# Kernel optimization log

Hardware: AMD Instinct MI355X
Metric: run time of the kernel (lower is better)

## Reference

```python
import jax, jax.numpy as jnp
import numpy as np

K = 3            # kernel_size
H = 2048
W = 2048
N = 1_000_000    # number of query points
LATENT = 4
POS = 6
CTRL = 2
HID = 64
OUT = 4
IN_CH = (LATENT + POS + CTRL) * K * K  # 108


def _linear_params(key, fan_in, fan_out):
    bound = 1.0 / np.sqrt(fan_in)
    kw, kb = jax.random.split(key)
    Wm = jax.random.uniform(kw, (fan_in, fan_out), minval=-bound, maxval=bound, dtype=jnp.float32)
    bm = jax.random.uniform(kb, (fan_out,), minval=-bound, maxval=bound, dtype=jnp.float32)
    return Wm, bm


def setup_inputs() -> dict:
    key = jax.random.key(0)
    ks = jax.random.split(key, 7)
    W1, b1 = _linear_params(ks[0], IN_CH, HID)
    W2, b2 = _linear_params(ks[1], HID, 2 * HID)
    W3, b3 = _linear_params(ks[2], 2 * HID, HID)
    W4, b4 = _linear_params(ks[3], HID, OUT)
    latent = jax.random.normal(ks[4], (H, W, LATENT), dtype=jnp.float32)
    raw_pos = jax.random.randint(ks[5], (N, 2), 0, W).astype(jnp.int32)  # (x, y) coords
    control = jax.random.normal(ks[6], (N, CTRL), dtype=jnp.float32)
    return {"latent": latent, "raw_pos": raw_pos, "control": control,
            "W1": W1, "b1": b1, "W2": W2, "b2": b2,
            "W3": W3, "b3": b3, "W4": W4, "b4": b4}


def reference(latent, raw_pos, control, W1, b1, W2, b2, W3, b3, W4, b4):
    Hh, Ww, C = latent.shape
    n = raw_pos.shape[0]
    r = K // 2
    d = jnp.arange(-r, r + 1, dtype=raw_pos.dtype)
    ox, oy = jnp.meshgrid(d, d, indexing="xy")
    offsets = jnp.stack([ox.ravel(), oy.ravel()], axis=-1)          # [K*K, 2] (dx, dy)
    exp = raw_pos[:, None, :] + offsets[None, :, :]                 # [N, K*K, 2]
    ex = jnp.clip(exp[..., 0], 0, Ww - 1)
    ey = jnp.clip(exp[..., 1], 0, Hh - 1)
    lin = ey * Ww + ex                                              # linear gather indices
    latent_values = latent.reshape(-1, C)[lin]                      # [N, K*K, C] irregular gather

    xs = jnp.clip(raw_pos[:, 0:1], 0, Ww - 1).astype(latent.dtype) / Ww
    ys = jnp.clip(raw_pos[:, 1:2], 0, Hh - 1).astype(latent.dtype) / Hh
    tp = jnp.asarray(2.0 * np.pi, latent.dtype)
    # sinusoidal encoding with input included: [x, y, sin(2pi x), cos(2pi x), sin(2pi y), cos(2pi y)] -> pos_channels=6
    pos = jnp.concatenate([xs, ys, jnp.sin(tp * xs), jnp.cos(tp * xs), jnp.sin(tp * ys), jnp.cos(tp * ys)], axis=-1)
    pos_e = jnp.broadcast_to(pos[:, None, :], (n, K * K, POS))
    ctl_e = jnp.broadcast_to(control[:, None, :], (n, K * K, control.shape[-1]))

    patches = jnp.concatenate([latent_values, pos_e, ctl_e], axis=-1)  # [N, K*K, 12]
    x = patches.reshape(n, -1)                                          # [N, 108]

    h = jax.nn.gelu(x @ W1 + b1, approximate=False)
    h = jax.nn.gelu(h @ W2 + b2, approximate=False)
    h = jax.nn.gelu(h @ W3 + b3, approximate=False)
    return jax.nn.sigmoid(h @ W4 + b4)                                  # [N, 4]
```

## Files before the change

### kernel.cpp

```cpp
#include <hip/hip_runtime.h>
#include <hip/hip_fp16.h>

typedef __attribute__((ext_vector_type(8))) _Float16 half8;
typedef __attribute__((ext_vector_type(4))) float f32x4;

#define HGT 2048
#define WID 2048
#define NPTS 1000000
#define NTILES 7813
#define WBYTES 44096
#define BIAS_OFF 43008
#define WAVE_BUF 4352
#define LDS_BYTES (WBYTES + 8*WAVE_BUF)
#define ROW_B 272

__global__ void prepack_kernel(const float* __restrict__ W1, const float* __restrict__ b1,
                               const float* __restrict__ W2, const float* __restrict__ b2,
                               const float* __restrict__ W3, const float* __restrict__ b3,
                               const float* __restrict__ W4, const float* __restrict__ b4,
                               unsigned short* __restrict__ packed){
  int tid = blockIdx.x*256 + threadIdx.x;
  if (tid < 42*64) {
    int f = tid >> 6, l = tid & 63;
    int row = l & 15, kgrp = l >> 4;
    int layer, nt, kk;
    if (f < 8)       { layer=1; nt=f>>1;      kk=f&1; }
    else if (f < 24) { layer=2; nt=(f-8)>>1;  kk=(f-8)&1; }
    else if (f < 40) { layer=3; nt=(f-24)>>2; kk=(f-24)&3; }
    else             { layer=4; nt=0;         kk=f-40; }
    unsigned short v16[8];
    #pragma unroll
    for (int e=0;e<8;e++){
      int k = kk*32 + kgrp*8 + e;
      int col = nt*16 + row;
      float v = 0.0f;
      if (layer==1) {
        if (k < 36)      { v = W1[((k>>2)*12 + (k&3))*64 + col]; }
        else if (k < 42) { float s=0.f; for (int p=0;p<9;p++) s += W1[(p*12+4+(k-36))*64 + col]; v=s; }
        else if (k < 44) { float s=0.f; for (int p=0;p<9;p++) s += W1[(p*12+10+(k-42))*64 + col]; v=s; }
      } else if (layer==2) { v = W2[k*128 + col]; }
      else if (layer==3)   { v = W3[k*64 + col]; }
      else                 { v = (col < 4) ? W4[k*4 + col] : 0.0f; }
      v16[e] = __half_as_ushort(__float2half(v));
    }
    unsigned short* dst = packed + (size_t)f*512 + (size_t)l*8;
    #pragma unroll
    for (int e=0;e<8;e++) dst[e] = v16[e];
  }
  int bt = tid - 42*64;
  if (bt >= 0 && bt < 272) {
    float v;
    if (bt < 64)       v = b1[bt];
    else if (bt < 192) v = b2[bt-64];
    else if (bt < 256) v = b3[bt-192];
    else               v = (bt-256 < 4) ? b4[bt-256] : 0.0f;
    ((float*)((char*)packed + BIAS_OFF))[bt] = v;
  }
}

__device__ inline unsigned gelu2_bits(float a, float b){
  __half2 x = __builtin_bit_cast(__half2, __builtin_amdgcn_cvt_pkrtz(a, b));
  const __half2 c0  = __float2half2_rn(2.3021164f);
  const __half2 c1  = __float2half2_rn(0.10294913f);
  const __half2 one = __float2half2_rn(1.0f);
  __half2 x2 = __hmul2(x, x);
  __half2 z  = __hmul2(x, __hfma2(c1, x2, c0));
  __half2 t  = h2exp2(z);
  __half2 r  = h2rcp(__hadd2(t, one));
  __half2 res = __hmul2(x, __hsub2(one, r));
  return __builtin_bit_cast(unsigned, res);
}
__device__ inline float fast_sigmoid(float x){
  return __builtin_amdgcn_rcpf(1.0f + __builtin_amdgcn_exp2f(-1.442695041f*x));
}

template<int MT, int KT, int FB, int BO>
__device__ inline void layer_fwd(const half8* __restrict__ Wfrag, const float* __restrict__ bias,
                                 char* hb, int nlo, int g, int lane){
  half8 bx[KT];
  #pragma unroll
  for (int kk=0; kk<KT; kk++)
    bx[kk] = *(const half8*)(hb + nlo*ROW_B + kk*64 + g*16);
  #pragma unroll
  for (int mt=0; mt<MT; mt++){
    f32x4 c = {0.f,0.f,0.f,0.f};
    #pragma unroll
    for (int kk=0; kk<KT; kk++)
      c = __builtin_amdgcn_mfma_f32_16x16x32_f16(Wfrag[(FB + mt*KT + kk)*64 + lane], bx[kk], c, 0,0,0);
    const f32x4 bv = *(const f32x4*)(bias + BO + mt*16 + g*4);
    uint2 w;
    w.x = gelu2_bits(c[0]+bv[0], c[1]+bv[1]);
    w.y = gelu2_bits(c[2]+bv[2], c[3]+bv[3]);
    *(uint2*)(hb + nlo*ROW_B + (mt*16 + g*4)*2) = w;
  }
}

__global__ __launch_bounds__(512, 4)
void decoder_kernel(const float* __restrict__ latent, const int* __restrict__ raw_pos,
                    const float* __restrict__ control, const unsigned short* __restrict__ packed,
                    float* __restrict__ out){
  extern __shared__ __attribute__((aligned(16))) char smem[];
  const int tid = threadIdx.x;
  {
    const f32x4* src = (const f32x4*)packed;
    f32x4* dst = (f32x4*)smem;
    for (int i = tid; i < WBYTES/16; i += 512) dst[i] = src[i];
    for (int i = tid; i < 128*5; i += 512) {
      int row = i / 5, p = i % 5;
      uint2 z; z.x = 0u; z.y = 0u;
      *(uint2*)(smem + WBYTES + (row>>4)*WAVE_BUF + (row&15)*ROW_B + 88 + p*8) = z;
    }
  }
  __syncthreads();

  const int wave = tid >> 6;
  const int lane = tid & 63;
  char* hb = smem + WBYTES + wave*WAVE_BUF;
  const half8* Wfrag = (const half8*)smem;
  const float* bias = (const float*)(smem + BIAS_OFF);
  const int row4 = lane >> 2;
  const int part = lane & 3;
  const int nlo  = lane & 15;
  const int g    = lane >> 4;

  for (int tile = blockIdx.x; tile < NTILES; tile += gridDim.x) {
    const int R0 = tile*128 + wave*16;
    if (R0 >= NPTS) continue;
    asm volatile("s_waitcnt lgkmcnt(0)" ::: "memory");
    {
      const int prow = R0 + row4;
      const int2 xy = ((const int2*)raw_pos)[prow];
      char* xrow = hb + row4*ROW_B;
      if (part < 3) {
        const int ey = min(max(xy.y + part - 1, 0), HGT-1);
        const float* lrow = latent + (size_t)ey * (WID*4);
        #pragma unroll
        for (int j=0;j<3;j++){
          const int ex = min(max(xy.x + j - 1, 0), WID-1);
          const float4 lv = *(const float4*)(lrow + (size_t)ex*4);
          uint2 pk;
          pk.x = __builtin_bit_cast(unsigned, __builtin_amdgcn_cvt_pkrtz(lv.x, lv.y));
          pk.y = __builtin_bit_cast(unsigned, __builtin_amdgcn_cvt_pkrtz(lv.z, lv.w));
          *(uint2*)(xrow + (part*3+j)*8) = pk;
        }
      } else {
        const float xs = (float)min(max(xy.x,0),WID-1) * (1.0f/WID);
        const float ys = (float)min(max(xy.y,0),HGT-1) * (1.0f/HGT);
        const float sx = __builtin_amdgcn_sinf(xs);
        const float cx = __builtin_amdgcn_cosf(xs);
        const float sy = __builtin_amdgcn_sinf(ys);
        const float cy = __builtin_amdgcn_cosf(ys);
        const float2 ct = ((const float2*)control)[prow];
        uint2 pa, pb;
        pa.x = __builtin_bit_cast(unsigned, __builtin_amdgcn_cvt_pkrtz(xs, ys));
        pa.y = __builtin_bit_cast(unsigned, __builtin_amdgcn_cvt_pkrtz(sx, cx));
        pb.x = __builtin_bit_cast(unsigned, __builtin_amdgcn_cvt_pkrtz(sy, cy));
        pb.y = __builtin_bit_cast(unsigned, __builtin_amdgcn_cvt_pkrtz(ct.x, ct.y));
        *(uint2*)(xrow + 72) = pa;
        *(uint2*)(xrow + 80) = pb;
      }
    }
    asm volatile("s_waitcnt lgkmcnt(0) vmcnt(0)" ::: "memory");

    layer_fwd<4, 2, 0,   0>(Wfrag, bias, hb, nlo, g, lane);
    asm volatile("s_waitcnt lgkmcnt(0)" ::: "memory");
    layer_fwd<8, 2, 8,  64>(Wfrag, bias, hb, nlo, g, lane);
    asm volatile("s_waitcnt lgkmcnt(0)" ::: "memory");
    layer_fwd<4, 4, 24, 192>(Wfrag, bias, hb, nlo, g, lane);
    asm volatile("s_waitcnt lgkmcnt(0)" ::: "memory");

    {
      half8 bx0 = *(const half8*)(hb + nlo*ROW_B +  0 + g*16);
      half8 bx1 = *(const half8*)(hb + nlo*ROW_B + 64 + g*16);
      f32x4 c = {0.f,0.f,0.f,0.f};
      c = __builtin_amdgcn_mfma_f32_16x16x32_f16(Wfrag[40*64 + lane], bx0, c, 0,0,0);
      c = __builtin_amdgcn_mfma_f32_16x16x32_f16(Wfrag[41*64 + lane], bx1, c, 0,0,0);
      const f32x4 bv = *(const f32x4*)(bias + 256 + g*4);
      if (g == 0) {
        f32x4 o;
        #pragma unroll
        for (int j=0;j<4;j++) o[j] = fast_sigmoid(c[j] + bv[j]);
        *(f32x4*)(out + (size_t)(R0 + nlo)*4) = o;
      }
    }
  }
}

extern "C" void kernel_launch(void* const* d_in, const int* in_sizes, int n_in,
                              void* d_out, int out_size, void* d_ws, size_t ws_size,
                              hipStream_t stream) {
  const float* latent  = (const float*)d_in[0];
  const int*   raw_pos = (const int*)d_in[1];
  const float* control = (const float*)d_in[2];
  const float* W1 = (const float*)d_in[3];
  const float* b1 = (const float*)d_in[4];
  const float* W2 = (const float*)d_in[5];
  const float* b2 = (const float*)d_in[6];
  const float* W3 = (const float*)d_in[7];
  const float* b3 = (const float*)d_in[8];
  const float* W4 = (const float*)d_in[9];
  const float* b4 = (const float*)d_in[10];
  unsigned short* packed = (unsigned short*)d_ws;

  static bool attr_set = false;
  if (!attr_set) {
    (void)hipFuncSetAttribute((const void*)decoder_kernel,
                              hipFuncAttributeMaxDynamicSharedMemorySize, LDS_BYTES);
    attr_set = true;
  }

  prepack_kernel<<<12, 256, 0, stream>>>(W1,b1,W2,b2,W3,b3,W4,b4,packed);
  decoder_kernel<<<1024, 512, LDS_BYTES, stream>>>(latent, raw_pos, control, packed, (float*)d_out);
}
```

Before: 120.0 us.

## Keep MLP activations in registers via permuted weight packing, drop LDS staging

```diff
diff --git a/kernel.cpp b/kernel.cpp
--- a/kernel.cpp
+++ b/kernel.cpp
@@ -3,16 +3,21 @@
 
 typedef __attribute__((ext_vector_type(8))) _Float16 half8;
 typedef __attribute__((ext_vector_type(4))) float f32x4;
+typedef __attribute__((ext_vector_type(4))) unsigned int uint4v;
 
 #define HGT 2048
 #define WID 2048
 #define NPTS 1000000
-#define NTILES 7813
+#define NTILES 3907
 #define WBYTES 44096
 #define BIAS_OFF 43008
-#define WAVE_BUF 4352
-#define LDS_BYTES (WBYTES + 8*WAVE_BUF)
-#define ROW_B 272
+
+__device__ __host__ inline int c64map(int k){
+  return 16*(k>>5) + 32*((k&7)>>2) + 4*((k>>3)&3) + (k&3);
+}
+__device__ __host__ inline int c128map(int k){
+  return 16*(k>>5) + 64*((k&7)>>2) + 4*((k>>3)&3) + (k&3);
+}
 
 __global__ void prepack_kernel(const float* __restrict__ W1, const float* __restrict__ b1,
                                const float* __restrict__ W2, const float* __restrict__ b2,
@@ -22,25 +27,25 @@
   int tid = blockIdx.x*256 + threadIdx.x;
   if (tid < 42*64) {
     int f = tid >> 6, l = tid & 63;
-    int row = l & 15, kgrp = l >> 4;
-    int layer, nt, kk;
-    if (f < 8)       { layer=1; nt=f>>1;      kk=f&1; }
-    else if (f < 24) { layer=2; nt=(f-8)>>1;  kk=(f-8)&1; }
-    else if (f < 40) { layer=3; nt=(f-24)>>2; kk=(f-24)&3; }
-    else             { layer=4; nt=0;         kk=f-40; }
+    int fr = l & 15, kg = l >> 4;
+    int layer, mt, kk;
+    if (f < 8)       { layer=1; mt=f>>1;      kk=f&1; }
+    else if (f < 24) { layer=2; mt=(f-8)>>1;  kk=(f-8)&1; }
+    else if (f < 40) { layer=3; mt=(f-24)>>2; kk=(f-24)&3; }
+    else             { layer=4; mt=0;         kk=f-40; }
     unsigned short v16[8];
     #pragma unroll
     for (int e=0;e<8;e++){
-      int k = kk*32 + kgrp*8 + e;
-      int col = nt*16 + row;
+      int k = kk*32 + kg*8 + e;
+      int fout = mt*16 + fr;
       float v = 0.0f;
       if (layer==1) {
-        if (k < 36)      { v = W1[((k>>2)*12 + (k&3))*64 + col]; }
-        else if (k < 42) { float s=0.f; for (int p=0;p<9;p++) s += W1[(p*12+4+(k-36))*64 + col]; v=s; }
-        else if (k < 44) { float s=0.f; for (int p=0;p<9;p++) s += W1[(p*12+10+(k-42))*64 + col]; v=s; }
-      } else if (layer==2) { v = W2[k*128 + col]; }
-      else if (layer==3)   { v = W3[k*64 + col]; }
-      else                 { v = (col < 4) ? W4[k*4 + col] : 0.0f; }
+        if (k < 36)      { v = W1[((k>>2)*12 + (k&3))*64 + fout]; }
+        else if (k < 42) { float s=0.f; for (int p=0;p<9;p++) s += W1[(p*12+4+(k-36))*64 + fout]; v=s; }
+        else if (k < 44) { float s=0.f; for (int p=0;p<9;p++) s += W1[(p*12+10+(k-42))*64 + fout]; v=s; }
+      } else if (layer==2) { v = W2[c64map(k)*128 + fout]; }
+      else if (layer==3)   { v = W3[c128map(k)*64 + fout]; }
+      else                 { v = (fr < 4) ? W4[c64map(k)*4 + fr] : 0.0f; }
       v16[e] = __half_as_ushort(__float2half(v));
     }
     unsigned short* dst = packed + (size_t)f*512 + (size_t)l*8;
@@ -58,6 +63,9 @@
   }
 }
 
+__device__ inline unsigned pkf(float a, float b){
+  return __builtin_bit_cast(unsigned, __builtin_amdgcn_cvt_pkrtz(a, b));
+}
 __device__ inline unsigned gelu2_bits(float a, float b){
   __half2 x = __builtin_bit_cast(__half2, __builtin_amdgcn_cvt_pkrtz(a, b));
   const __half2 c0  = __float2half2_rn(2.3021164f);
@@ -73,115 +81,116 @@
 __device__ inline float fast_sigmoid(float x){
   return __builtin_amdgcn_rcpf(1.0f + __builtin_amdgcn_exp2f(-1.442695041f*x));
 }
-
-template<int MT, int KT, int FB, int BO>
-__device__ inline void layer_fwd(const half8* __restrict__ Wfrag, const float* __restrict__ bias,
-                                 char* hb, int nlo, int g, int lane){
-  half8 bx[KT];
-  #pragma unroll
-  for (int kk=0; kk<KT; kk++)
-    bx[kk] = *(const half8*)(hb + nlo*ROW_B + kk*64 + g*16);
+__device__ inline half8 mk8(uint2 a, uint2 b){
+  uint4v t; t.x = a.x; t.y = a.y; t.z = b.x; t.w = b.y;
+  return __builtin_bit_cast(half8, t);
+}
+
+template<int MT,int KT,int FB,int BO>
+__device__ inline void layer2(const half8* __restrict__ Wfrag, const float* __restrict__ bias,
+                              const half8* bxa, const half8* bxb,
+                              uint2* ua, uint2* ub, int lane, int g){
   #pragma unroll
   for (int mt=0; mt<MT; mt++){
-    f32x4 c = {0.f,0.f,0.f,0.f};
-    #pragma unroll
-    for (int kk=0; kk<KT; kk++)
-      c = __builtin_amdgcn_mfma_f32_16x16x32_f16(Wfrag[(FB + mt*KT + kk)*64 + lane], bx[kk], c, 0,0,0);
     const f32x4 bv = *(const f32x4*)(bias + BO + mt*16 + g*4);
-    uint2 w;
-    w.x = gelu2_bits(c[0]+bv[0], c[1]+bv[1]);
-    w.y = gelu2_bits(c[2]+bv[2], c[3]+bv[3]);
-    *(uint2*)(hb + nlo*ROW_B + (mt*16 + g*4)*2) = w;
-  }
-}
-
-__global__ __launch_bounds__(512, 4)
+    f32x4 a = bv, b = bv;
+    #pragma unroll
+    for (int kk=0; kk<KT; kk++){
+      const half8 w = Wfrag[(FB + mt*KT + kk)*64 + lane];
+      a = __builtin_amdgcn_mfma_f32_16x16x32_f16(w, bxa[kk], a, 0,0,0);
+      b = __builtin_amdgcn_mfma_f32_16x16x32_f16(w, bxb[kk], b, 0,0,0);
+    }
+    ua[mt].x = gelu2_bits(a[0], a[1]); ua[mt].y = gelu2_bits(a[2], a[3]);
+    ub[mt].x = gelu2_bits(b[0], b[1]); ub[mt].y = gelu2_bits(b[2], b[3]);
+  }
+}
+
+__global__ __launch_bounds__(512, 6)
 void decoder_kernel(const float* __restrict__ latent, const int* __restrict__ raw_pos,
                     const float* __restrict__ control, const unsigned short* __restrict__ packed,
                     float* __restrict__ out){
-  extern __shared__ __attribute__((aligned(16))) char smem[];
+  __shared__ __attribute__((aligned(16))) char smem[WBYTES];
   const int tid = threadIdx.x;
   {
     const f32x4* src = (const f32x4*)packed;
     f32x4* dst = (f32x4*)smem;
     for (int i = tid; i < WBYTES/16; i += 512) dst[i] = src[i];
-    for (int i = tid; i < 128*5; i += 512) {
-      int row = i / 5, p = i % 5;
-      uint2 z; z.x = 0u; z.y = 0u;
-      *(uint2*)(smem + WBYTES + (row>>4)*WAVE_BUF + (row&15)*ROW_B + 88 + p*8) = z;
-    }
   }
   __syncthreads();
 
-  const int wave = tid >> 6;
-  const int lane = tid & 63;
-  char* hb = smem + WBYTES + wave*WAVE_BUF;
   const half8* Wfrag = (const half8*)smem;
-  const float* bias = (const float*)(smem + BIAS_OFF);
-  const int row4 = lane >> 2;
-  const int part = lane & 3;
-  const int nlo  = lane & 15;
-  const int g    = lane >> 4;
-
-  for (int tile = blockIdx.x; tile < NTILES; tile += gridDim.x) {
-    const int R0 = tile*128 + wave*16;
+  const float* bias  = (const float*)(smem + BIAS_OFF);
+  const int wave = tid >> 6, lane = tid & 63;
+  const int nlo = lane & 15, g = lane >> 4;
+  const int pA = g*2, pB = g*2+1;
+  const int qA = (pA>=3) + (pA>=6), qB = (pB>=3) + (pB>=6);
+  const int dyA = qA-1, dxA = pA-3*qA-1;
+  const int dyB = qB-1, dxB = pB-3*qB-1;
+
+  for (int tile = blockIdx.x; tile < NTILES; tile += gridDim.x){
+    const int R0 = tile*256 + wave*32;
     if (R0 >= NPTS) continue;
-    asm volatile("s_waitcnt lgkmcnt(0)" ::: "memory");
-    {
-      const int prow = R0 + row4;
+
+    half8 bx[2][2];
+    #pragma unroll
+    for (int jj=0; jj<2; jj++){
+      const int prow = R0 + jj*16 + nlo;
       const int2 xy = ((const int2*)raw_pos)[prow];
-      char* xrow = hb + row4*ROW_B;
-      if (part < 3) {
-        const int ey = min(max(xy.y + part - 1, 0), HGT-1);
-        const float* lrow = latent + (size_t)ey * (WID*4);
-        #pragma unroll
-        for (int j=0;j<3;j++){
-          const int ex = min(max(xy.x + j - 1, 0), WID-1);
-          const float4 lv = *(const float4*)(lrow + (size_t)ex*4);
-          uint2 pk;
-          pk.x = __builtin_bit_cast(unsigned, __builtin_amdgcn_cvt_pkrtz(lv.x, lv.y));
-          pk.y = __builtin_bit_cast(unsigned, __builtin_amdgcn_cvt_pkrtz(lv.z, lv.w));
-          *(uint2*)(xrow + (part*3+j)*8) = pk;
-        }
-      } else {
-        const float xs = (float)min(max(xy.x,0),WID-1) * (1.0f/WID);
-        const float ys = (float)min(max(xy.y,0),HGT-1) * (1.0f/HGT);
-        const float sx = __builtin_amdgcn_sinf(xs);
-        const float cx = __builtin_amdgcn_cosf(xs);
-        const float sy = __builtin_amdgcn_sinf(ys);
-        const float cy = __builtin_amdgcn_cosf(ys);
+      const int exA = min(max(xy.x + dxA, 0), WID-1);
+      const int eyA = min(max(xy.y + dyA, 0), HGT-1);
+      const int exB = min(max(xy.x + dxB, 0), WID-1);
+      const int eyB = min(max(xy.y + dyB, 0), HGT-1);
+      const f32x4 lA = *(const f32x4*)(latent + ((size_t)eyA*WID + exA)*4);
+      const f32x4 lB = *(const f32x4*)(latent + ((size_t)eyB*WID + exB)*4);
+      uint4v f0;
+      f0.x = pkf(lA[0], lA[1]); f0.y = pkf(lA[2], lA[3]);
+      f0.z = pkf(lB[0], lB[1]); f0.w = pkf(lB[2], lB[3]);
+      bx[jj][0] = __builtin_bit_cast(half8, f0);
+
+      const float xs = (float)xy.x * (1.0f/WID), ys = (float)xy.y * (1.0f/HGT);
+      const float sx = __builtin_amdgcn_sinf(xs), cx = __builtin_amdgcn_cosf(xs);
+      const float sy = __builtin_amdgcn_sinf(ys), cy = __builtin_amdgcn_cosf(ys);
+      uint4v f1; f1.x = 0u; f1.y = 0u; f1.z = 0u; f1.w = 0u;
+      if (g == 0){
+        const int ex8 = min(xy.x + 1, WID-1), ey8 = min(xy.y + 1, HGT-1);
+        const f32x4 l8 = *(const f32x4*)(latent + ((size_t)ey8*WID + ex8)*4);
+        f1.x = pkf(l8[0], l8[1]); f1.y = pkf(l8[2], l8[3]);
+        f1.z = pkf(xs, ys); f1.w = pkf(sx, cx);
+      } else if (g == 1){
         const float2 ct = ((const float2*)control)[prow];
-        uint2 pa, pb;
-        pa.x = __builtin_bit_cast(unsigned, __builtin_amdgcn_cvt_pkrtz(xs, ys));
-        pa.y = __builtin_bit_cast(unsigned, __builtin_amdgcn_cvt_pkrtz(sx, cx));
-        pb.x = __builtin_bit_cast(unsigned, __builtin_amdgcn_cvt_pkrtz(sy, cy));
-        pb.y = __builtin_bit_cast(unsigned, __builtin_amdgcn_cvt_pkrtz(ct.x, ct.y));
-        *(uint2*)(xrow + 72) = pa;
-        *(uint2*)(xrow + 80) = pb;
+        f1.x = pkf(sy, cy); f1.y = pkf(ct.x, ct.y);
       }
-    }
-    asm volatile("s_waitcnt lgkmcnt(0) vmcnt(0)" ::: "memory");
-
-    layer_fwd<4, 2, 0,   0>(Wfrag, bias, hb, nlo, g, lane);
-    asm volatile("s_waitcnt lgkmcnt(0)" ::: "memory");
-    layer_fwd<8, 2, 8,  64>(Wfrag, bias, hb, nlo, g, lane);
-    asm volatile("s_waitcnt lgkmcnt(0)" ::: "memory");
-    layer_fwd<4, 4, 24, 192>(Wfrag, bias, hb, nlo, g, lane);
-    asm volatile("s_waitcnt lgkmcnt(0)" ::: "memory");
-
-    {
-      half8 bx0 = *(const half8*)(hb + nlo*ROW_B +  0 + g*16);
-      half8 bx1 = *(const half8*)(hb + nlo*ROW_B + 64 + g*16);
-      f32x4 c = {0.f,0.f,0.f,0.f};
-      c = __builtin_amdgcn_mfma_f32_16x16x32_f16(Wfrag[40*64 + lane], bx0, c, 0,0,0);
-      c = __builtin_amdgcn_mfma_f32_16x16x32_f16(Wfrag[41*64 + lane], bx1, c, 0,0,0);
-      const f32x4 bv = *(const f32x4*)(bias + 256 + g*4);
-      if (g == 0) {
-        f32x4 o;
-        #pragma unroll
-        for (int j=0;j<4;j++) o[j] = fast_sigmoid(c[j] + bv[j]);
-        *(f32x4*)(out + (size_t)(R0 + nlo)*4) = o;
-      }
+      bx[jj][1] = __builtin_bit_cast(half8, f1);
+    }
+
+    uint2 u0[8], u1[8];
+    half8 ha[4], hb[4];
+    layer2<4,2,0,0>(Wfrag, bias, bx[0], bx[1], u0, u1, lane, g);
+    ha[0]=mk8(u0[0],u0[2]); ha[1]=mk8(u0[1],u0[3]);
+    hb[0]=mk8(u1[0],u1[2]); hb[1]=mk8(u1[1],u1[3]);
+    layer2<8,2,8,64>(Wfrag, bias, ha, hb, u0, u1, lane, g);
+    ha[0]=mk8(u0[0],u0[4]); ha[1]=mk8(u0[1],u0[5]);
+    ha[2]=mk8(u0[2],u0[6]); ha[3]=mk8(u0[3],u0[7]);
+    hb[0]=mk8(u1[0],u1[4]); hb[1]=mk8(u1[1],u1[5]);
+    hb[2]=mk8(u1[2],u1[6]); hb[3]=mk8(u1[3],u1[7]);
+    layer2<4,4,24,192>(Wfrag, bias, ha, hb, u0, u1, lane, g);
+    ha[0]=mk8(u0[0],u0[2]); ha[1]=mk8(u0[1],u0[3]);
+    hb[0]=mk8(u1[0],u1[2]); hb[1]=mk8(u1[1],u1[3]);
+
+    const f32x4 bv4 = *(const f32x4*)(bias + 256 + g*4);
+    f32x4 a = bv4, b = bv4;
+    #pragma unroll
+    for (int kk=0; kk<2; kk++){
+      const half8 w = Wfrag[(40+kk)*64 + lane];
+      a = __builtin_amdgcn_mfma_f32_16x16x32_f16(w, ha[kk], a, 0,0,0);
+      b = __builtin_amdgcn_mfma_f32_16x16x32_f16(w, hb[kk], b, 0,0,0);
+    }
+    if (g == 0){
+      f32x4 oa, ob;
+      #pragma unroll
+      for (int j=0;j<4;j++){ oa[j] = fast_sigmoid(a[j]); ob[j] = fast_sigmoid(b[j]); }
+      *(f32x4*)(out + (size_t)(R0 + nlo)*4)      = oa;
+      *(f32x4*)(out + (size_t)(R0 + 16 + nlo)*4) = ob;
     }
   }
 }
@@ -202,13 +211,6 @@
   const float* b4 = (const float*)d_in[10];
   unsigned short* packed = (unsigned short*)d_ws;
 
-  static bool attr_set = false;
-  if (!attr_set) {
-    (void)hipFuncSetAttribute((const void*)decoder_kernel,
-                              hipFuncAttributeMaxDynamicSharedMemorySize, LDS_BYTES);
-    attr_set = true;
-  }
-
   prepack_kernel<<<12, 256, 0, stream>>>(W1,b1,W2,b2,W3,b3,W4,b4,packed);
-  decoder_kernel<<<1024, 512, LDS_BYTES, stream>>>(latent, raw_pos, control, packed, (float*)d_out);
-}
+  decoder_kernel<<<NTILES, 512, 0, stream>>>(latent, raw_pos, control, packed, (float*)d_out);
+}
```

Result: faster. 109.3 us (-8.9%).
